# Kernel optimization log

Hardware: AMD Instinct MI355X
Metric: run time of the kernel (lower is better)

Reference implementation:

```python
import jax, jax.numpy as jnp
import numpy as np

N_HEADS = 16
COORDS = 1024
K_DIM = COORDS // N_HEADS  # 64


def setup_inputs() -> dict:
    key = jax.random.key(0)
    k1, k2, k3, k4 = jax.random.split(key, 4)
    x = jax.random.normal(k1, (2, 2048, COORDS), dtype=jnp.float32)
    W_proj = jax.random.normal(k2, (COORDS, COORDS), dtype=jnp.float32) * 0.02
    pre_metric = jax.random.normal(k3, (N_HEADS, K_DIM, K_DIM), dtype=jnp.float32) + jnp.eye(K_DIM, dtype=jnp.float32) * 0.01
    W_mix = jax.random.normal(k4, (COORDS, COORDS), dtype=jnp.float32) * 0.02
    return {"in_sequence_bwc": x, "W_proj": W_proj, "pre_metric": pre_metric, "W_mix": W_mix}


def reference(in_sequence_bwc, W_proj, pre_metric, W_mix):
    b, w, c = in_sequence_bwc.shape
    n, k = N_HEADS, K_DIM
    neg_inf = jnp.float32(-jnp.inf)
    sqrt_k = jnp.sqrt(jnp.float32(k))

    # build per-head metric: lower-tri mask on pre_metric, row softmax, then P @ P^T
    tril_kk = jnp.tril(jnp.ones((k, k), dtype=bool))
    pm_nkk = jnp.where(tril_kk, pre_metric, neg_inf)
    pm_nkk = jax.nn.softmax(pm_nkk / sqrt_k, axis=-1)
    metric_nkk = pm_nkk @ jnp.swapaxes(pm_nkk, -1, -2)

    # shared projection used as Q, K and V (torch Linear: x @ W.T, no bias)
    proj_bwc = in_sequence_bwc @ W_proj.T
    proj_bnwk = proj_bwc.reshape(b, w, n, k).transpose(0, 2, 1, 3)  # [b,n,w,k]

    # bilinear scores: Q @ M @ K^T, scaled
    qm_bnwk = jnp.einsum('bnik,nkl->bnil', proj_bnwk, metric_nkk)
    scores_bnww = jnp.einsum('bnik,bnjk->bnij', qm_bnwk, proj_bnwk) / sqrt_k

    causal_ww = jnp.tril(jnp.ones((w, w), dtype=bool))
    scores_bnww = jnp.where(causal_ww[None, None], scores_bnww, neg_inf)
    att_bnww = jax.nn.softmax(scores_bnww, axis=-1)

    nudged_bnwk = att_bnww @ proj_bnwk
    nudged_bwc = nudged_bnwk.transpose(0, 2, 1, 3).reshape(b, w, c)
    return nudged_bwc @ W_mix.T
```

## Files before the change

### kernel.cpp

```cpp
#include <hip/hip_runtime.h>
#include <stdint.h>
#include <stddef.h>

typedef unsigned short u16;
typedef unsigned int u32;
typedef __attribute__((ext_vector_type(8))) __bf16 bf16x8;
typedef __attribute__((ext_vector_type(4))) float f32x4;
typedef __attribute__((ext_vector_type(16))) float f32x16;

#define DEV __device__ __forceinline__

#define BATCH 2
#define SEQ   2048
#define CDIM  1024
#define NH    16
#define KD    64
#define MROWS (BATCH * SEQ)
#define NX (MROWS * CDIM)
#define NW (CDIM * CDIM)
#define BHSZ  131072

DEV u16 f32_to_bf16(float f) {
  union { float f; unsigned u; } v; v.f = f;
  return (u16)((v.u + 0x7fffu + ((v.u >> 16) & 1u)) >> 16);
}
DEV u32 pack_bf16x2(float a, float b) {
  union { __bf16 h[2]; u32 u; } r;
  r.h[0] = (__bf16)a; r.h[1] = (__bf16)b;
  return r.u;
}
DEV u32 pack_trunc(float a, float b) {
  return __builtin_amdgcn_perm(__float_as_uint(b), __float_as_uint(a), 0x07060302u);
}
DEV float v_exp2(float x) {
  float r; asm("v_exp_f32 %0, %1" : "=v"(r) : "v"(x)); return r;
}

DEV void gl_lds16(const u16* g, u16* l) {
  __builtin_amdgcn_global_load_lds(
      (const __attribute__((address_space(1))) void*)(g),
      (__attribute__((address_space(3))) void*)(l), 16, 0, 0);
}


__global__ void cvt_metric(const float* __restrict__ x, const float* __restrict__ wp,
                           const float* __restrict__ wm, const float* __restrict__ pm,
                           u16* __restrict__ xb, u16* __restrict__ wpb,
                           u16* __restrict__ wmb, u16* __restrict__ metric) {
  __shared__ float P[64][65];
  int bid = blockIdx.x, t = threadIdx.x;
  if (bid < 2048) {
    int total4 = (NX + 2 * NW) >> 2;
    for (int i4 = bid * 256 + t; i4 < total4; i4 += 2048 * 256) {
      int i = i4 << 2;
      const float* src; u16* dst; int off;
      if (i < NX)           { src = x;  dst = xb;  off = i; }
      else if (i < NX + NW) { src = wp; dst = wpb; off = i - NX; }
      else                  { src = wm; dst = wmb; off = i - NX - NW; }
      float4 v = *reinterpret_cast<const float4*>(src + off);
      uint2 o;
      o.x = pack_trunc(v.x, v.y);
      o.y = pack_trunc(v.z, v.w);
      *reinterpret_cast<uint2*>(dst + off) = o;
    }
    return;
  }
  int mb = bid - 2048;
  int h = mb >> 4, jgrp = mb & 15;
  if (t < 64) {
    int i = t;
    const float* row = pm + (size_t)(h * 64 + i) * 64;
    float mx = -1e30f;
    for (int j = 0; j <= i; ++j) mx = fmaxf(mx, row[j] * 0.125f);
    float s = 0.f;
    for (int j = 0; j <= i; ++j) { float e = expf(row[j] * 0.125f - mx); P[i][j] = e; s += e; }
    float inv = 1.f / s;
    for (int j = 0; j <= i; ++j) P[i][j] *= inv;
    for (int j = i + 1; j < 64; ++j) P[i][j] = 0.f;
  }
  __syncthreads();
  {
    int i = t & 63, jq = t >> 6;
    int j = jgrp * 4 + jq;
    float acc = 0.f;
    #pragma unroll
    for (int l = 0; l < 64; ++l) acc += P[i][l] * P[j][l];
    metric[(size_t)h * 4096 + i * 64 + j] = f32_to_bf16(acc);
  }
}

template <int MODE>
__launch_bounds__(256)
__global__ void gemm_xwt(const u16* __restrict__ A, const u16* __restrict__ B,
                         void* __restrict__ C0, u16* __restrict__ C1,
                         const u16* __restrict__ Mbf, u16* __restrict__ Qf,
                         int M, int N, int K) {
  __shared__ __align__(16) u16 SM[2 * 12288];
  int bm0 = blockIdx.x * 128, bn0 = blockIdx.y * 64;
  int t = threadIdx.x, wv = t >> 6, lane = t & 63;
  int l15 = lane & 15, l4 = lane >> 4;
  f32x4 acc[2][4] = {};

  const int r8 = lane >> 3;
  const int sseg = ((lane & 7) ^ r8) * 8;

  auto stage = [&](int k0, u16* dst) {
    #pragma unroll
    for (int q = 0; q < 4; ++q) {
      int rowl = q * 32 + wv * 8;
      gl_lds16(A + (size_t)(bm0 + rowl + r8) * K + k0 + sseg, dst + rowl * 64);
    }
    u16* dstB = dst + 8192;
    #pragma unroll
    for (int q = 0; q < 2; ++q) {
      int rowl = q * 32 + wv * 8;
      gl_lds16(B + (size_t)(bn0 + rowl + r8) * K + k0 + sseg, dstB + rowl * 64);
    }
  };

  stage(0, SM);
  __syncthreads();
  const int NKS = K >> 6;
  for (int ks = 0; ks < NKS; ++ks) {
    u16* cur = SM + (ks & 1) * 12288;
    if (ks + 1 < NKS) stage((ks + 1) * 64, SM + ((ks + 1) & 1) * 12288);
    const u16* As = cur;
    const u16* Bs = cur + 8192;
    #pragma unroll
    for (int kk = 0; kk < 2; ++kk) {
      bf16x8 af[2], bfm[4];
      #pragma unroll
      for (int m = 0; m < 2; ++m) {
        int R = wv * 32 + m * 16 + l15;
        af[m] = *reinterpret_cast<const bf16x8*>(As + R * 64 + ((kk * 4 + l4) ^ (R & 7)) * 8);
      }
      #pragma unroll
      for (int nn = 0; nn < 4; ++nn) {
        int R = nn * 16 + l15;
        bfm[nn] = *reinterpret_cast<const bf16x8*>(Bs + R * 64 + ((kk * 4 + l4) ^ (R & 7)) * 8);
      }
      #pragma unroll
      for (int m = 0; m < 2; ++m)
        #pragma unroll
        for (int nn = 0; nn < 4; ++nn)
          acc[m][nn] = __builtin_amdgcn_mfma_f32_16x16x32_bf16(af[m], bfm[nn], acc[m][nn], 0, 0, 0);
    }
    __syncthreads();
  }

  if (MODE == 0) {
    int h = bn0 >> 6, bb = bm0 >> 11;
    size_t base = (size_t)(bb * NH + h) * BHSZ;
    u16* Pl = SM;
    u16* Ml = SM + 9216;
    #pragma unroll
    for (int it = 0; it < 2; ++it) {
      int i = t * 8 + it * 2048;
      int r = i >> 6, c8 = i & 63;
      *reinterpret_cast<uint4*>(Ml + r * 72 + c8) =
          *reinterpret_cast<const uint4*>(Mbf + h * 4096 + i);
    }
    #pragma unroll
    for (int m = 0; m < 2; ++m) {
      #pragma unroll
      for (int nn = 0; nn < 4; ++nn) {
        u16 hv4[4];
        #pragma unroll
        for (int rr = 0; rr < 4; ++rr) {
          int rowl = wv * 32 + m * 16 + l4 * 4 + rr;
          int d = nn * 16 + l15;
          u16 hv = f32_to_bf16(acc[m][nn][rr]);
          hv4[rr] = hv;
          int w2 = (bm0 & 2047) + rowl;
          int tile = w2 >> 6, rt = w2 & 63;
          int rl = rt & 31;
          int rls = (rl & 19) | ((rl & 4) << 1) | ((rl & 8) >> 1);
          ((u16*)C0)[base + (size_t)(tile * 8 + (d >> 4) * 2 + (rt >> 5)) * 512
                     + (rls | (((d >> 3) & 1) << 5)) * 8 + (d & 7)] = hv;
          Pl[rowl * 72 + d] = hv;
        }
        {
          int rowl0 = wv * 32 + m * 16 + l4 * 4;
          int d = nn * 16 + l15;
          int w20 = (bm0 & 2047) + rowl0;
          int tile = w20 >> 6, rt0 = w20 & 63;
          uint2 vv;
          vv.x = (u32)hv4[0] | ((u32)hv4[1] << 16);
          vv.y = (u32)hv4[2] | ((u32)hv4[3] << 16);
          *reinterpret_cast<uint2*>(
              C1 + base + (size_t)(tile * 8 + ((rt0 >> 4) & 3) * 2 + (d >> 5)) * 512
                 + ((d & 31) | (((rt0 >> 3) & 1) << 5)) * 8 + (rt0 & 7)) = vv;
        }
      }
    }
    __syncthreads();
    const float cl2 = 0.125f * 1.44269504088896f;
    f32x4 acc2[2][4] = {};
    #pragma unroll
    for (int kk2 = 0; kk2 < 2; ++kk2) {
      bf16x8 af2[2], bm2[4];
      #pragma unroll
      for (int m = 0; m < 2; ++m)
        af2[m] = *reinterpret_cast<const bf16x8*>(Pl + (wv * 32 + m * 16 + l15) * 72 + kk2 * 32 + l4 * 8);
      #pragma unroll
      for (int nn = 0; nn < 4; ++nn)
        bm2[nn] = *reinterpret_cast<const bf16x8*>(Ml + (nn * 16 + l15) * 72 + kk2 * 32 + l4 * 8);
      #pragma unroll
      for (int m = 0; m < 2; ++m)
        #pragma unroll
        for (int nn = 0; nn < 4; ++nn)
          acc2[m][nn] = __builtin_amdgcn_mfma_f32_16x16x32_bf16(af2[m], bm2[nn], acc2[m][nn], 0, 0, 0);
    }
    #pragma unroll
    for (int m = 0; m < 2; ++m) {
      #pragma unroll
      for (int nn = 0; nn < 4; ++nn) {
        #pragma unroll
        for (int rr = 0; rr < 4; ++rr) {
          int rowl = wv * 32 + m * 16 + l4 * 4 + rr;
          int d = nn * 16 + l15;
          int w2 = (bm0 & 2047) + rowl;
          Qf[base + (size_t)((w2 >> 5) * 4 + (d >> 4)) * 512
             + ((w2 & 31) | (((d >> 3) & 1) << 5)) * 8 + (d & 7)]
              = f32_to_bf16(acc2[m][nn][rr] * cl2);
        }
      }
    }
  } else {
    #pragma unroll
    for (int m = 0; m < 2; ++m) {
      int rbase = bm0 + wv * 32 + m * 16 + l4 * 4;
      #pragma unroll
      for (int nn = 0; nn < 4; ++nn) {
        int col = bn0 + nn * 16 + l15;
        #pragma unroll
        for (int rr = 0; rr < 4; ++rr)
          ((float*)C0)[(size_t)(rbase + rr) * N + col] = acc[m][nn][rr];
      }
    }
  }
}

__launch_bounds__(256, 4)
__global__ void attn_kernel(const u16* __restrict__ Qf, const u16* __restrict__ Kf,
                            const u16* __restrict__ Vf, u16* __restrict__ nudged) {
  const int bh = blockIdx.x;
  const int bb = bh >> 4, h = bh & 15;
  const int p = 63 - (int)blockIdx.y;
  const int t = threadIdx.x, wv = t >> 6, lane = t & 63;
  const int c = lane & 31, hi = lane >> 5;
  const int q0 = p * 32;

  __shared__ float smf[4][2176];

  const u16* __restrict__ Kbh = Kf + (size_t)bh * BHSZ;
  const u16* __restrict__ Vbh = Vf + (size_t)bh * BHSZ;

  bf16x8 qf[4];
  {
    const u16* __restrict__ Qb = Qf + (size_t)bh * BHSZ + p * 2048 + lane * 8;
    #pragma unroll
    for (int kc = 0; kc < 4; ++kc)
      qf[kc] = *reinterpret_cast<const bf16x8*>(Qb + kc * 512);
  }

  f32x16 o0 = {}, o1 = {};
  float sv0 = 0.f, sv1 = 0.f;

  const int half = wv & 1;
  u32 koff = (u32)((wv >> 1) * 4096 + half * 512 + lane * 8);
  u32 voff = (u32)((wv >> 1) * 4096 + half * 2048 + lane * 8);

  bf16x8 kf[4], vf0[2], vf1[2];
  if (wv <= p) {
    #pragma unroll
    for (int kc = 0; kc < 4; ++kc)
      kf[kc] = *reinterpret_cast<const bf16x8*>(Kbh + koff + kc * 1024);
    #pragma unroll
    for (int ksl = 0; ksl < 2; ++ksl) {
      vf0[ksl] = *reinterpret_cast<const bf16x8*>(Vbh + voff + ksl * 1024);
      vf1[ksl] = *reinterpret_cast<const bf16x8*>(Vbh + voff + ksl * 1024 + 512);
    }
  }

  for (int T = wv; T <= p; T += 4) {
    f32x16 s = {};
    __builtin_amdgcn_s_setprio(1);
    #pragma unroll
    for (int kc = 0; kc < 4; ++kc)
      s = __builtin_amdgcn_mfma_f32_32x32x16_bf16(kf[kc], qf[kc], s, 0, 0, 0);
    __builtin_amdgcn_s_setprio(0);
    if (T + 4 <= p) {
      #pragma unroll
      for (int kc = 0; kc < 4; ++kc)
        kf[kc] = *reinterpret_cast<const bf16x8*>(Kbh + koff + 8192 + kc * 1024);
    }
    if (T == p) {
      #pragma unroll
      for (int r = 0; r < 16; ++r) {
        int kvl = (r & 3) + 4 * ((r >> 2) & 1) + 8 * hi + 16 * (r >> 3);
        if (kvl > c) s[r] = -1e30f;
      }
    }
    #pragma unroll
    for (int ksl = 0; ksl < 2; ++ksl) {
      float a = v_exp2(s[ksl * 8 + 0]);
      float b = v_exp2(s[ksl * 8 + 1]);
      float cc = v_exp2(s[ksl * 8 + 2]);
      float d = v_exp2(s[ksl * 8 + 3]);
      float e = v_exp2(s[ksl * 8 + 4]);
      float f = v_exp2(s[ksl * 8 + 5]);
      float g2 = v_exp2(s[ksl * 8 + 6]);
      float h2 = v_exp2(s[ksl * 8 + 7]);
      union { u32 u[4]; bf16x8 v; } pk;
      pk.u[0] = pack_trunc(a, b);
      pk.u[1] = pack_trunc(cc, d);
      pk.u[2] = pack_trunc(e, f);
      pk.u[3] = pack_trunc(g2, h2);
      __builtin_amdgcn_s_setprio(1);
      o0 = __builtin_amdgcn_mfma_f32_32x32x16_bf16(vf0[ksl], pk.v, o0, 0, 0, 0);
      o1 = __builtin_amdgcn_mfma_f32_32x32x16_bf16(vf1[ksl], pk.v, o1, 0, 0, 0);
      __builtin_amdgcn_s_setprio(0);
      sv0 += (a + b) + (cc + d);
      sv1 += (e + f) + (g2 + h2);
    }
    if (T + 4 <= p) {
      #pragma unroll
      for (int ksl = 0; ksl < 2; ++ksl) {
        vf0[ksl] = *reinterpret_cast<const bf16x8*>(Vbh + voff + 8192 + ksl * 1024);
        vf1[ksl] = *reinterpret_cast<const bf16x8*>(Vbh + voff + 8192 + ksl * 1024 + 512);
      }
    }
    koff += 8192; voff += 8192;
  }

  float lrow;
  {
    float s2 = sv0 + sv1;
    lrow = s2 + __shfl_xor(s2, 32);
  }

  {
    float* Ob = smf[wv];
    #pragma unroll
    for (int r = 0; r < 16; ++r) {
      int d = (r & 3) + 8 * (r >> 2) + 4 * hi;
      Ob[d * 33 + c] = o0[r];
      Ob[(d + 32) * 33 + c] = o1[r];
    }
    if (hi == 0) Ob[2112 + c] = lrow;
  }
  __syncthreads();
  {
    int q = t >> 3, dseg = t & 7;
    float lsum = smf[0][2112 + q] + smf[1][2112 + q] + smf[2][2112 + q] + smf[3][2112 + q];
    float invd = 1.f / lsum;
    u16 outv[8];
    #pragma unroll
    for (int i2 = 0; i2 < 8; ++i2) {
      int d = dseg * 8 + i2;
      float v = smf[0][d * 33 + q] + smf[1][d * 33 + q] + smf[2][d * 33 + q] + smf[3][d * 33 + q];
      outv[i2] = f32_to_bf16(v * invd);
    }
    u16* dstp = nudged + ((size_t)bb * SEQ + q0 + q) * CDIM + h * KD + dseg * 8;
    uint4 ov;
    ov.x = (u32)outv[0] | ((u32)outv[1] << 16);
    ov.y = (u32)outv[2] | ((u32)outv[3] << 16);
    ov.z = (u32)outv[4] | ((u32)outv[5] << 16);
    ov.w = (u32)outv[6] | ((u32)outv[7] << 16);
    *reinterpret_cast<uint4*>(dstp) = ov;
  }
}

extern "C" void kernel_launch(void* const* d_in, const int* in_sizes, int n_in,
                              void* d_out, int out_size, void* d_ws, size_t ws_size,
                              hipStream_t stream) {
  (void)in_sizes; (void)n_in; (void)out_size; (void)ws_size;
  const float* x      = (const float*)d_in[0];
  const float* Wproj  = (const float*)d_in[1];
  const float* premet = (const float*)d_in[2];
  const float* Wmix   = (const float*)d_in[3];

  char* w = (char*)d_ws;
  u16* x_bf   = (u16*)w;  w += (size_t)MROWS * CDIM * 2;
  u16* wp_bf  = (u16*)w;  w += (size_t)CDIM * CDIM * 2;
  u16* wm_bf  = (u16*)w;  w += (size_t)CDIM * CDIM * 2;
  u16* metric = (u16*)w;  w += (size_t)NH * KD * KD * 2;
  u16* Kf     = (u16*)w;  w += (size_t)BATCH * NH * BHSZ * 2;
  u16* Vf     = (u16*)w;  w += (size_t)BATCH * NH * BHSZ * 2;
  u16* Qf     = (u16*)w;  w += (size_t)BATCH * NH * BHSZ * 2;
  u16* nudged = (u16*)w;  w += (size_t)MROWS * CDIM * 2;

  hipLaunchKernelGGL(cvt_metric, dim3(2304), dim3(256), 0, stream,
                     x, Wproj, Wmix, premet, x_bf, wp_bf, wm_bf, metric);
  hipLaunchKernelGGL((gemm_xwt<0>), dim3(MROWS / 128, CDIM / 64), dim3(256), 0, stream,
                     x_bf, wp_bf, (void*)Kf, Vf, metric, Qf, MROWS, CDIM, CDIM);
  hipLaunchKernelGGL(attn_kernel, dim3(32, 64), dim3(256), 0, stream,
                     Qf, Kf, Vf, nudged);
  hipLaunchKernelGGL((gemm_xwt<1>), dim3(MROWS / 128, CDIM / 64), dim3(256), 0, stream,
                     nudged, wm_bf, d_out, nullptr, nullptr, nullptr, MROWS, CDIM, CDIM);
}
```

Baseline: 86.16 us.

## Fuse fp32-to-bf16 conversion of x into projection GEMM A-tile staging

The projection GEMM now reads x directly as fp32 into registers, converts to bf16 and writes the swizzled tile to LDS after the MFMA loop, instead of relying on a separate pre-pass that wrote a bf16 copy of x. The conversion kernel now only handles the two weight matrices and the metric. This removes a full read and write of the 16 MB activation through global memory. In exchange, the A operand is loaded at twice the bytes per tile through registers instead of async global-to-LDS loads, which raises register pressure and can expose load latency.

```diff
diff --git a/kernel.cpp b/kernel.cpp
--- a/kernel.cpp
+++ b/kernel.cpp
@@ -43,20 +43,19 @@
 }
 
 
-__global__ void cvt_metric(const float* __restrict__ x, const float* __restrict__ wp,
-                           const float* __restrict__ wm, const float* __restrict__ pm,
-                           u16* __restrict__ xb, u16* __restrict__ wpb,
-                           u16* __restrict__ wmb, u16* __restrict__ metric) {
+__global__ void cvt_metric(const float* __restrict__ wp, const float* __restrict__ wm,
+                           const float* __restrict__ pm,
+                           u16* __restrict__ wpb, u16* __restrict__ wmb,
+                           u16* __restrict__ metric) {
   __shared__ float P[64][65];
   int bid = blockIdx.x, t = threadIdx.x;
-  if (bid < 2048) {
-    int total4 = (NX + 2 * NW) >> 2;
-    for (int i4 = bid * 256 + t; i4 < total4; i4 += 2048 * 256) {
+  if (bid < 512) {
+    int total4 = (2 * NW) >> 2;
+    for (int i4 = bid * 256 + t; i4 < total4; i4 += 512 * 256) {
       int i = i4 << 2;
       const float* src; u16* dst; int off;
-      if (i < NX)           { src = x;  dst = xb;  off = i; }
-      else if (i < NX + NW) { src = wp; dst = wpb; off = i - NX; }
-      else                  { src = wm; dst = wmb; off = i - NX - NW; }
+      if (i < NW) { src = wp; dst = wpb; off = i; }
+      else        { src = wm; dst = wmb; off = i - NW; }
       float4 v = *reinterpret_cast<const float4*>(src + off);
       uint2 o;
       o.x = pack_trunc(v.x, v.y);
@@ -65,7 +64,7 @@
     }
     return;
   }
-  int mb = bid - 2048;
+  int mb = bid - 512;
   int h = mb >> 4, jgrp = mb & 15;
   if (t < 64) {
     int i = t;
@@ -103,13 +102,39 @@
 
   const int r8 = lane >> 3;
   const int sseg = ((lane & 7) ^ r8) * 8;
-
-  auto stage = [&](int k0, u16* dst) {
+  const float* Af = reinterpret_cast<const float*>(A);
+
+  float4 va[4][2];
+
+  auto ldA0 = [&](int k0) {
+    #pragma unroll
+    for (int q = 0; q < 4; ++q) {
+      int rowf = q * 32 + wv * 8 + r8;
+      const float* src = Af + (size_t)(bm0 + rowf) * K + k0 + (lane & 7) * 8;
+      va[q][0] = *reinterpret_cast<const float4*>(src);
+      va[q][1] = *reinterpret_cast<const float4*>(src + 4);
+    }
+  };
+  auto stA0 = [&](u16* dst) {
+    #pragma unroll
+    for (int q = 0; q < 4; ++q) {
+      int rowf = q * 32 + wv * 8 + r8;
+      uint4 pk4;
+      pk4.x = pack_trunc(va[q][0].x, va[q][0].y);
+      pk4.y = pack_trunc(va[q][0].z, va[q][0].w);
+      pk4.z = pack_trunc(va[q][1].x, va[q][1].y);
+      pk4.w = pack_trunc(va[q][1].z, va[q][1].w);
+      *reinterpret_cast<uint4*>(dst + rowf * 64 + sseg) = pk4;
+    }
+  };
+  auto stageA1 = [&](int k0, u16* dst) {
     #pragma unroll
     for (int q = 0; q < 4; ++q) {
       int rowl = q * 32 + wv * 8;
       gl_lds16(A + (size_t)(bm0 + rowl + r8) * K + k0 + sseg, dst + rowl * 64);
     }
+  };
+  auto stageB = [&](int k0, u16* dst) {
     u16* dstB = dst + 8192;
     #pragma unroll
     for (int q = 0; q < 2; ++q) {
@@ -118,12 +143,17 @@
     }
   };
 
-  stage(0, SM);
+  if (MODE == 0) { ldA0(0); stageB(0, SM); stA0(SM); }
+  else           { stageA1(0, SM); stageB(0, SM); }
   __syncthreads();
   const int NKS = K >> 6;
   for (int ks = 0; ks < NKS; ++ks) {
     u16* cur = SM + (ks & 1) * 12288;
-    if (ks + 1 < NKS) stage((ks + 1) * 64, SM + ((ks + 1) & 1) * 12288);
+    u16* nxt = SM + ((ks + 1) & 1) * 12288;
+    if (ks + 1 < NKS) {
+      if (MODE == 0) { ldA0((ks + 1) * 64); stageB((ks + 1) * 64, nxt); }
+      else           { stageA1((ks + 1) * 64, nxt); stageB((ks + 1) * 64, nxt); }
+    }
     const u16* As = cur;
     const u16* Bs = cur + 8192;
     #pragma unroll
@@ -145,6 +175,7 @@
         for (int nn = 0; nn < 4; ++nn)
           acc[m][nn] = __builtin_amdgcn_mfma_f32_16x16x32_bf16(af[m], bfm[nn], acc[m][nn], 0, 0, 0);
     }
+    if (MODE == 0 && ks + 1 < NKS) stA0(nxt);
     __syncthreads();
   }
 
@@ -382,7 +413,6 @@
   const float* Wmix   = (const float*)d_in[3];
 
   char* w = (char*)d_ws;
-  u16* x_bf   = (u16*)w;  w += (size_t)MROWS * CDIM * 2;
   u16* wp_bf  = (u16*)w;  w += (size_t)CDIM * CDIM * 2;
   u16* wm_bf  = (u16*)w;  w += (size_t)CDIM * CDIM * 2;
   u16* metric = (u16*)w;  w += (size_t)NH * KD * KD * 2;
@@ -391,10 +421,10 @@
   u16* Qf     = (u16*)w;  w += (size_t)BATCH * NH * BHSZ * 2;
   u16* nudged = (u16*)w;  w += (size_t)MROWS * CDIM * 2;
 
-  hipLaunchKernelGGL(cvt_metric, dim3(2304), dim3(256), 0, stream,
-                     x, Wproj, Wmix, premet, x_bf, wp_bf, wm_bf, metric);
+  hipLaunchKernelGGL(cvt_metric, dim3(768), dim3(256), 0, stream,
+                     Wproj, Wmix, premet, wp_bf, wm_bf, metric);
   hipLaunchKernelGGL((gemm_xwt<0>), dim3(MROWS / 128, CDIM / 64), dim3(256), 0, stream,
-                     x_bf, wp_bf, (void*)Kf, Vf, metric, Qf, MROWS, CDIM, CDIM);
+                     (const u16*)x, wp_bf, (void*)Kf, Vf, metric, Qf, MROWS, CDIM, CDIM);
   hipLaunchKernelGGL(attn_kernel, dim3(32, 64), dim3(256), 0, stream,
                      Qf, Kf, Vf, nudged);
   hipLaunchKernelGGL((gemm_xwt<1>), dim3(MROWS / 128, CDIM / 64), dim3(256), 0, stream,
```

Result: no change. 87.49 us (+1.5%).
